# Performance work log

Hardware: AMD Instinct MI355X
Metric: run time of the kernel (lower is better)

## Reference

```python
import jax, jax.numpy as jnp
import numpy as np

S, D, BN, GH, AH, FCH = 18, 512, 32, 128, 16, 512


def setup_inputs() -> dict:
    key = jax.random.key(0)
    ks = jax.random.split(key, 20)
    B = 8192
    sc = 0.05
    inp = {
        "local_styles": jax.random.normal(ks[0], (B, S, D), jnp.float32),
        "global_styles": jax.random.normal(ks[1], (B, S, D), jnp.float32),
        "target_ages": jax.random.uniform(ks[2], (B,), jnp.float32),
        # per-style bottleneck MLPs (512->32->32), stacked over styles
        "bn_w1": jax.random.normal(ks[3], (S, D, BN), jnp.float32) * sc,
        "bn_b1": jnp.zeros((S, BN), jnp.float32),
        "bn_w2": jax.random.normal(ks[4], (S, BN, BN), jnp.float32) * sc,
        "bn_b2": jnp.zeros((S, BN), jnp.float32),
        # global mlp (18*32 -> 128 -> 128)
        "gm_w1": jax.random.normal(ks[5], (S * BN, GH), jnp.float32) * sc,
        "gm_b1": jnp.zeros((GH,), jnp.float32),
        "gm_w2": jax.random.normal(ks[6], (GH, GH), jnp.float32) * sc,
        "gm_b2": jnp.zeros((GH,), jnp.float32),
        # age mlp (1 -> 16 -> 16)
        "age_w1": jax.random.normal(ks[7], (1, AH), jnp.float32) * sc,
        "age_b1": jnp.zeros((AH,), jnp.float32),
        "age_w2": jax.random.normal(ks[8], (AH, AH), jnp.float32) * sc,
        "age_b2": jnp.zeros((AH,), jnp.float32),
        # per-style fc MLPs (128+16+512 -> 512 -> 512), stacked over styles
        "fc_w1": jax.random.normal(ks[9], (S, GH + AH + D, FCH), jnp.float32) * sc,
        "fc_b1": jnp.zeros((S, FCH), jnp.float32),
        "fc_w2": jax.random.normal(ks[10], (S, FCH, D), jnp.float32) * sc,
        "fc_b2": jnp.zeros((S, D), jnp.float32),
    }
    return inp


def reference(local_styles, global_styles, target_ages,
              bn_w1, bn_b1, bn_w2, bn_b2,
              gm_w1, gm_b1, gm_w2, gm_b2,
              age_w1, age_b1, age_w2, age_b2,
              fc_w1, fc_b1, fc_w2, fc_b2):
    B = global_styles.shape[0]
    # per-style bottlenecks as batched GEMMs over the style axis
    h = jax.nn.relu(jnp.einsum('bsd,sdk->bsk', global_styles, bn_w1) + bn_b1)
    h = jnp.einsum('bsk,skm->bsm', h, bn_w2) + bn_b2          # [B, S, 32]
    gf = h.reshape(B, S * BN)                                  # concat over styles
    gf = jax.nn.relu(gf @ gm_w1 + gm_b1) @ gm_w2 + gm_b2      # [B, 128]
    af = target_ages[:, None]                                  # [B, 1]
    af = jax.nn.relu(af @ age_w1 + age_b1) @ age_w2 + age_b2   # [B, 16]
    gfa = jnp.concatenate([gf, af], axis=1)                    # [B, 144]
    # per-style fc: input is [global_feats, style_i] -> [B, S, 656]
    x = jnp.concatenate([jnp.broadcast_to(gfa[:, None, :], (B, S, GH + AH)),
                         global_styles], axis=2)
    y = jax.nn.relu(jnp.einsum('bsf,sfh->bsh', x, fc_w1) + fc_b1)
    y = jnp.einsum('bsh,shd->bsd', y, fc_w2) + fc_b2
    return y + global_styles
```

## Files before the change

### kernel.cpp

```cpp
#include <hip/hip_runtime.h>

typedef unsigned short u16;
typedef unsigned int   u32;
typedef __attribute__((ext_vector_type(4))) float floatx4;
typedef __attribute__((ext_vector_type(8))) short shortx8;

#define BB 8192
#define SS 18
#define DD 512

__device__ __forceinline__ u16 f2bf(float f){
  u32 u = __float_as_uint(f);
  return (u16)((u + 0x7FFFu + ((u >> 16) & 1u)) >> 16);
}
__device__ __forceinline__ float bf2f(u16 x){ return __uint_as_float(((u32)x)<<16); }

__device__ __forceinline__ shortx8 pack8v(floatx4 a, floatx4 b){
  shortx8 t;
  t[0]=(short)f2bf(a[0]); t[1]=(short)f2bf(a[1]); t[2]=(short)f2bf(a[2]); t[3]=(short)f2bf(a[3]);
  t[4]=(short)f2bf(b[0]); t[5]=(short)f2bf(b[1]); t[6]=(short)f2bf(b[2]); t[7]=(short)f2bf(b[3]);
  return t;
}

__device__ __forceinline__ void gload16(const void* g, void* l){
  __builtin_amdgcn_global_load_lds((const __attribute__((address_space(1))) void*)g,
                                   (__attribute__((address_space(3))) void*)l, 16, 0, 0);
}

template<int CALLS>
__device__ __forceinline__ void gstage(const char* src, size_t rowStrideB, int chunkByteOff,
                                       char* lds, int wid, int lane){
#pragma unroll
  for (int i=0;i<CALLS;++i){
    int base = (wid*CALLS + i)*1024;
    int off  = base + lane*16;
    int row  = off >> 7;
    int blk  = ((off >> 4) & 7) ^ (row & 7);
    gload16(src + (size_t)row*rowStrideB + chunkByteOff + blk*16, lds + base);
  }
}

__device__ __forceinline__ void lds_store4(char* buf, int row, int rowBytes, int khByte,
                                           int swzMask, const shortx8* v){
#pragma unroll
  for (int q=0;q<4;++q){
    int off = row*rowBytes + khByte + q*16;
    off ^= (row & swzMask) << 4;
    *(shortx8*)(buf + off) = v[q];
  }
}

__device__ __forceinline__ void stage_bf16(char* buf, const u16* gsrc, size_t srcRowBytes, int tid){
  int row = tid >> 1, kh = tid & 1;
  const char* p = (const char*)gsrc + (size_t)row*srcRowBytes + kh*64;
  shortx8 v[4];
#pragma unroll
  for (int q=0;q<4;++q) v[q] = *(const shortx8*)(p + q*16);
  lds_store4(buf, row, 128, kh*64, 7, v);
}

__device__ __forceinline__ shortx8 lds_frag(const char* buf, int row, int rowBytes, int kByte,
                                            int swzMask, int lane){
  int off = row*rowBytes + kByte + ((lane>>4)<<4);
  off ^= (row & swzMask) << 4;
  return *(const shortx8*)(buf + off);
}

template<int MF, int NF>
__device__ __forceinline__ void mma64(const char* As, const char* Bs, int wm, int wn, int lane,
                                      floatx4 acc[MF][NF]){
#pragma unroll
  for (int kk=0; kk<2; ++kk){
    shortx8 a[MF], b[NF];
#pragma unroll
    for (int i=0;i<MF;++i) a[i] = lds_frag(As, wm + i*16 + (lane&15), 128, kk*64, 7, lane);
#pragma unroll
    for (int j=0;j<NF;++j) b[j] = lds_frag(Bs, wn + j*16 + (lane&15), 128, kk*64, 7, lane);
#pragma unroll
    for (int i=0;i<MF;++i)
#pragma unroll
      for (int j=0;j<NF;++j)
        acc[i][j] = __builtin_amdgcn_mfma_f32_16x16x32_bf16(a[i], b[j], acc[i][j], 0, 0, 0);
  }
}

template<int MF, int NF>
__device__ __forceinline__ void frags_load(const char* As, const char* Bs, int wm, int wn, int lane,
                                           shortx8 a[2][MF], shortx8 b[2][NF]){
#pragma unroll
  for (int kk=0;kk<2;++kk){
#pragma unroll
    for (int i=0;i<MF;++i) a[kk][i] = lds_frag(As, wm + i*16 + (lane&15), 128, kk*64, 7, lane);
#pragma unroll
    for (int j=0;j<NF;++j) b[kk][j] = lds_frag(Bs, wn + j*16 + (lane&15), 128, kk*64, 7, lane);
  }
}
template<int MF, int NF>
__device__ __forceinline__ void frags_mma(shortx8 a[2][MF], shortx8 b[2][NF], floatx4 acc[MF][NF]){
#pragma unroll
  for (int kk=0;kk<2;++kk)
#pragma unroll
    for (int i=0;i<MF;++i)
#pragma unroll
      for (int j=0;j<NF;++j)
        acc[i][j] = __builtin_amdgcn_mfma_f32_16x16x32_bf16(a[kk][i], b[kk][j], acc[i][j], 0, 0, 0);
}

__device__ __forceinline__ int xcd_swz(int bid, int nwg){
  int q = nwg >> 3;
  return (bid & 7)*q + (bid >> 3);
}

__global__ __launch_bounds__(256) void transpose_w2(const float* __restrict__ src,
                                                    u16* __restrict__ dst,
                                                    int sKstride, int kSrcOff, int Kuse,
                                                    int N, int Kpad, int kDstOff){
  __shared__ float tile[32][33];
  int s = blockIdx.z;
  int k0 = blockIdx.x*32, n0 = blockIdx.y*32;
  int tx = threadIdx.x & 31, ty = threadIdx.x >> 5;
#pragma unroll
  for (int r=0;r<4;++r){
    int k = k0 + ty*4 + r;
    float v = (k < Kuse) ? src[((size_t)s*sKstride + kSrcOff + k)*N + n0 + tx] : 0.f;
    tile[ty*4+r][tx] = v;
  }
  __syncthreads();
#pragma unroll
  for (int r=0;r<4;++r){
    int n = n0 + ty*4 + r;
    dst[((size_t)s*N + n)*Kpad + kDstOff + k0 + tx] = f2bf(tile[tx][ty*4+r]);
  }
}

__global__ __launch_bounds__(256) void k_bn(const float* __restrict__ gs,
     const u16* __restrict__ w1t, const u16* __restrict__ w2t,
     const float* __restrict__ b1, const float* __restrict__ b2,
     u16* __restrict__ h2b, u16* __restrict__ gsb){
  __shared__ __align__(16) char SMB[40960];
  int tid = threadIdx.x, lane = tid & 63, wid = tid >> 6;
  int nb = xcd_swz(blockIdx.x, 1152);
  int m0 = (nb & 63)*128, s = nb >> 6;
  floatx4 acc[2][2] = {};
  const char*  Bsrc = (const char*)w1t + (size_t)s*32*1024;
  size_t rowIdx = ((size_t)(m0 + (tid>>1))*SS + s)*DD + (tid&1)*32;
  const float* Ags  = gs + rowIdx;
  u16*         Gsb  = gsb + rowIdx;
  floatx4 fr[8];
  gstage<1>(Bsrc, 1024, 0, SMB+32768, wid, lane);
#pragma unroll
  for (int q=0;q<8;++q) fr[q] = *(const floatx4*)(Ags + q*4);
  for (int c=0;c<8;++c){
    char* Asc = SMB + (c&1)*16384;
    char* Bsc = SMB + 32768 + (c&1)*4096;
    { shortx8 v[4];
#pragma unroll
      for (int q=0;q<4;++q) v[q] = pack8v(fr[2*q], fr[2*q+1]);
      u16* gp = Gsb + c*64;
#pragma unroll
      for (int q=0;q<4;++q) *(shortx8*)(gp + q*8) = v[q];
      lds_store4(Asc, tid>>1, 128, (tid&1)*64, 7, v); }
    __syncthreads();
    int cn = c+1;
    if (cn < 8){
      gstage<1>(Bsrc, 1024, cn*128, SMB + 32768 + (cn&1)*4096, wid, lane);
      const float* p = Ags + cn*64;
#pragma unroll
      for (int q=0;q<8;++q) fr[q] = *(const floatx4*)(p + q*4);
    }
    mma64<2,2>(Asc, Bsc, wid*32, 0, lane, acc);
  }
  __syncthreads();
  char* G1  = SMB;
  char* W2s = SMB + 8192;
#pragma unroll
  for (int i=0;i<2;++i)
#pragma unroll
   for (int j=0;j<2;++j){
    int col = j*16 + (lane&15);
    float bias = b1[s*32 + col];
#pragma unroll
    for (int r=0;r<4;++r){
      int row = wid*32 + i*16 + ((lane>>4)<<2) + r;
      float v = fmaxf(acc[i][j][r] + bias, 0.f);
      int off = (row*64 + col*2) ^ ((row&3)<<4);
      *(u16*)(G1 + off) = f2bf(v);
    }
  }
  if (tid < 32){
    const u16* p = w2t + (size_t)s*32*32 + tid*32;
#pragma unroll
    for (int q=0;q<4;++q){
      int off = (tid*64 + q*16) ^ ((tid&3)<<4);
      *(shortx8*)(W2s + off) = *(const shortx8*)(p + q*8);
    }
  }
  __syncthreads();
  floatx4 acc2[2][2] = {};
  {
    shortx8 a[2], b[2];
#pragma unroll
    for (int i=0;i<2;++i) a[i] = lds_frag(G1,  wid*32 + i*16 + (lane&15), 64, 0, 3, lane);
#pragma unroll
    for (int j=0;j<2;++j) b[j] = lds_frag(W2s, j*16 + (lane&15),          64, 0, 3, lane);
#pragma unroll
    for (int i=0;i<2;++i)
#pragma unroll
      for (int j=0;j<2;++j)
        acc2[i][j] = __builtin_amdgcn_mfma_f32_16x16x32_bf16(a[i], b[j], acc2[i][j], 0,0,0);
  }
#pragma unroll
  for (int i=0;i<2;++i)
#pragma unroll
   for (int j=0;j<2;++j){
    int col = j*16 + (lane&15);
    float bias = b2[s*32 + col];
#pragma unroll
    for (int r=0;r<4;++r){
      int row = wid*32 + i*16 + ((lane>>4)<<2) + r;
      h2b[((size_t)(m0+row)*SS + s)*32 + col] = f2bf(acc2[i][j][r] + bias);
    }
  }
}

__global__ __launch_bounds__(256) void k_gm(const u16* __restrict__ h2b,
     const u16* __restrict__ w1t, const u16* __restrict__ w2t,
     const float* __restrict__ b1, const float* __restrict__ b2,
     const float* __restrict__ ta, const float* __restrict__ aw1, const float* __restrict__ ab1,
     const float* __restrict__ aw2, const float* __restrict__ ab2,
     u16* __restrict__ gfab){
  __shared__ __align__(16) char As[128*128];
  __shared__ __align__(16) char Bs[128*128];
  __shared__ __align__(16) char G1[128*256];
  int tid=threadIdx.x, lane=tid&63, w=tid>>6;
  int m0 = blockIdx.x*128;
  floatx4 acc[2][8] = {};
  for (int c=0;c<9;++c){
    __syncthreads();
    stage_bf16(As, h2b + (size_t)m0*576 + c*64, 1152, tid);
    stage_bf16(Bs, w1t + c*64,                 1152, tid);
    __syncthreads();
    mma64<2,8>(As, Bs, w*32, 0, lane, acc);
  }
#pragma unroll
  for (int i=0;i<2;++i)
#pragma unroll
   for (int j=0;j<8;++j){
    int col = j*16 + (lane&15);
    float bias = b1[col];
#pragma unroll
    for (int r=0;r<4;++r){
      int row = w*32 + i*16 + ((lane>>4)<<2) + r;
      float v = fmaxf(acc[i][j][r] + bias, 0.f);
      int off = (row*256 + col*2) ^ ((row&7)<<4);
      *(u16*)(G1 + off) = f2bf(v);
    }
  }
  floatx4 acc2[2][8] = {};
  for (int c2=0;c2<2;++c2){
    __syncthreads();
    stage_bf16(Bs, w2t + c2*64, 256, tid);
    __syncthreads();
#pragma unroll
    for (int kk=0;kk<2;++kk){
      shortx8 a[2], b[8];
#pragma unroll
      for (int i=0;i<2;++i){
        int row = w*32 + i*16 + (lane&15);
        int off = (row*256 + c2*128 + kk*64 + ((lane>>4)<<4)) ^ ((row&7)<<4);
        a[i] = *(const shortx8*)(G1 + off);
      }
#pragma unroll
      for (int j=0;j<8;++j) b[j] = lds_frag(Bs, j*16 + (lane&15), 128, kk*64, 7, lane);
#pragma unroll
      for (int i=0;i<2;++i)
#pragma unroll
        for (int j=0;j<8;++j)
          acc2[i][j] = __builtin_amdgcn_mfma_f32_16x16x32_bf16(a[i], b[j], acc2[i][j], 0,0,0);
    }
  }
#pragma unroll
  for (int i=0;i<2;++i)
#pragma unroll
   for (int j=0;j<8;++j){
    int col = j*16 + (lane&15);
    float bias = b2[col];
#pragma unroll
    for (int r=0;r<4;++r){
      int row = w*32 + i*16 + ((lane>>4)<<2) + r;
      gfab[(size_t)(m0+row)*192 + col] = f2bf(acc2[i][j][r] + bias);
    }
  }
  if (tid < 128){
    int bidx = m0 + tid;
    float t = ta[bidx];
    float a1[16];
#pragma unroll
    for (int j2=0;j2<16;++j2){ float v = t*aw1[j2] + ab1[j2]; a1[j2] = fmaxf(v, 0.f); }
#pragma unroll
    for (int m=0;m<16;++m){
      float v = ab2[m];
#pragma unroll
      for (int j2=0;j2<16;++j2) v += a1[j2]*aw2[j2*16+m];
      gfab[(size_t)bidx*192 + 128 + m] = f2bf(v);
    }
    shortx8 zz = {};
#pragma unroll
    for (int z=0;z<6;++z) *(shortx8*)(gfab + (size_t)bidx*192 + 144 + z*8) = zz;
  }
}

__global__ __launch_bounds__(256) void k_fc1(const u16* __restrict__ gfab,
     const u16* __restrict__ gsb, const u16* __restrict__ w1t,
     const float* __restrict__ b1, u16* __restrict__ y1b){
  __shared__ __align__(16) char SMB[81920];
  int tid=threadIdx.x, lane=tid&63, wid=tid>>6;
  int nb = xcd_swz(blockIdx.x, 4608);
  int n0=(nb&3)*128, m0=((nb>>2)&63)*128, s=nb>>8;
  int wm=(wid>>1)*64, wn=(wid&1)*64;
  floatx4 acc[4][4] = {};
  const char* Ag   = (const char*)gfab + (size_t)m0*384;
  const char* Agl  = (const char*)gsb + ((size_t)m0*SS + s)*1024;
  const char* Bsrc = (const char*)w1t + ((size_t)s*512+n0)*1408;
#define F1_ISSA(t) do{ int _t=(t); char* _d = SMB + (_t%3)*16384; \
    if (_t<3) gstage<4>(Ag, 384, _t*128, _d, wid, lane); \
    else      gstage<4>(Agl, (size_t)SS*1024, _t*128-384, _d, wid, lane); }while(0)
#define F1_ISSB(t) gstage<4>(Bsrc, 1408, (t)*128, SMB+49152+((t)&1)*16384, wid, lane)
  F1_ISSB(0); F1_ISSA(0); F1_ISSA(1);
#pragma unroll 1
  for (int c=0;c<11;++c){
    if (c<10) asm volatile("s_waitcnt vmcnt(4)" ::: "memory");
    else      asm volatile("s_waitcnt vmcnt(0)" ::: "memory");
    __builtin_amdgcn_s_barrier();
    __builtin_amdgcn_sched_barrier(0);
    shortx8 a[2][4], b[2][4];
    frags_load<4,4>(SMB+(c%3)*16384, SMB+49152+(c&1)*16384, wm, wn, lane, a, b);
    if (c+1<11) F1_ISSB(c+1);
    if (c+2<11) F1_ISSA(c+2);
    frags_mma<4,4>(a, b, acc);
  }
  __syncthreads();
  char* OT = SMB;
#pragma unroll
  for (int i=0;i<4;++i)
#pragma unroll
   for (int j=0;j<4;++j){
    int col = wn + j*16 + (lane&15);
    float bias = b1[(size_t)s*512 + n0 + col];
#pragma unroll
    for (int r=0;r<4;++r){
      int row = wm + i*16 + ((lane>>4)<<2) + r;
      float v = fmaxf(acc[i][j][r] + bias, 0.f);
      int off = (row*256 + col*2) ^ ((row&7)<<4);
      *(u16*)(OT + off) = f2bf(v);
    }
  }
  __syncthreads();
  {
    int row = tid>>1, half = tid&1;
    u16* gp = y1b + ((size_t)(m0+row)*SS + s)*DD + n0 + half*64;
#pragma unroll
    for (int q=0;q<8;++q){
      int off = (row*256 + half*128 + q*16) ^ ((row&7)<<4);
      *(shortx8*)(gp + q*8) = *(const shortx8*)(OT + off);
    }
  }
}

__global__ __launch_bounds__(256) void k_fc2(const u16* __restrict__ y1b,
     const u16* __restrict__ gsb, const u16* __restrict__ w2t,
     const float* __restrict__ b2, float* __restrict__ out){
  __shared__ __align__(16) char SMB[81920];
  int tid=threadIdx.x, lane=tid&63, wid=tid>>6;
  int nb = xcd_swz(blockIdx.x, 4608);
  int n0=(nb&3)*128, m0=((nb>>2)&63)*128, s=nb>>8;
  int wm=(wid>>1)*64, wn=(wid&1)*64;
  floatx4 acc[4][4] = {};
  const char* Asrc = (const char*)y1b + ((size_t)m0*SS + s)*1024;
  const char* Bsrc = (const char*)w2t + ((size_t)s*512 + n0)*1024;
#define F2_ISSA(t) gstage<4>(Asrc, (size_t)SS*1024, (t)*128, SMB+((t)%3)*16384, wid, lane)
#define F2_ISSB(t) gstage<4>(Bsrc, 1024, (t)*128, SMB+49152+((t)&1)*16384, wid, lane)
  F2_ISSB(0); F2_ISSA(0); F2_ISSA(1);
#pragma unroll 1
  for (int c=0;c<8;++c){
    if (c<7) asm volatile("s_waitcnt vmcnt(4)" ::: "memory");
    else     asm volatile("s_waitcnt vmcnt(0)" ::: "memory");
    __builtin_amdgcn_s_barrier();
    __builtin_amdgcn_sched_barrier(0);
    shortx8 a[2][4], b[2][4];
    frags_load<4,4>(SMB+(c%3)*16384, SMB+49152+(c&1)*16384, wm, wn, lane, a, b);
    if (c+1<8) F2_ISSB(c+1);
    if (c+2<8) F2_ISSA(c+2);
    frags_mma<4,4>(a, b, acc);
  }
  __syncthreads();
  float* SMF = (float*)SMB;
#pragma unroll
  for (int i=0;i<4;++i)
#pragma unroll
   for (int j=0;j<4;++j){
    int col = wn + j*16 + (lane&15);
#pragma unroll
    for (int r=0;r<4;++r){
      int row = wm + i*16 + ((lane>>4)<<2) + r;
      int off = (row*512 + col*4) ^ ((row&7)<<4);
      *(float*)((char*)SMF + off) = acc[i][j][r];
    }
  }
  __syncthreads();
  {
    int row = tid>>1, half = tid&1;
    size_t gidx = ((size_t)(m0+row)*SS + s)*DD + n0 + half*64;
    const float* bp = b2 + (size_t)s*512 + n0 + half*64;
    const u16*   gp = gsb + gidx;
#pragma unroll
    for (int q2=0;q2<8;++q2){
      shortx8 gv = *(const shortx8*)(gp + q2*8);
      int off0 = (row*512 + half*256 + (2*q2)*16)   ^ ((row&7)<<4);
      int off1 = (row*512 + half*256 + (2*q2+1)*16) ^ ((row&7)<<4);
      floatx4 v0 = *(const floatx4*)((char*)SMF + off0);
      floatx4 v1 = *(const floatx4*)((char*)SMF + off1);
      floatx4 b0 = *(const floatx4*)(bp + q2*8);
      floatx4 b1v= *(const floatx4*)(bp + q2*8 + 4);
      floatx4 g0, g1;
      g0[0]=bf2f((u16)gv[0]); g0[1]=bf2f((u16)gv[1]); g0[2]=bf2f((u16)gv[2]); g0[3]=bf2f((u16)gv[3]);
      g1[0]=bf2f((u16)gv[4]); g1[1]=bf2f((u16)gv[5]); g1[2]=bf2f((u16)gv[6]); g1[3]=bf2f((u16)gv[7]);
      *(floatx4*)(out + gidx + q2*8)     = v0 + b0 + g0;
      *(floatx4*)(out + gidx + q2*8 + 4) = v1 + b1v + g1;
    }
  }
}

extern "C" void kernel_launch(void* const* d_in, const int* in_sizes, int n_in,
                              void* d_out, int out_size, void* d_ws, size_t ws_size,
                              hipStream_t stream){
  (void)in_sizes; (void)n_in; (void)out_size; (void)ws_size;
  const float* gs   = (const float*)d_in[1];
  const float* ta   = (const float*)d_in[2];
  const float* bnw1 = (const float*)d_in[3];
  const float* bnb1 = (const float*)d_in[4];
  const float* bnw2 = (const float*)d_in[5];
  const float* bnb2 = (const float*)d_in[6];
  const float* gmw1 = (const float*)d_in[7];
  const float* gmb1 = (const float*)d_in[8];
  const float* gmw2 = (const float*)d_in[9];
  const float* gmb2 = (const float*)d_in[10];
  const float* aw1  = (const float*)d_in[11];
  const float* ab1  = (const float*)d_in[12];
  const float* aw2  = (const float*)d_in[13];
  const float* ab2  = (const float*)d_in[14];
  const float* fcw1 = (const float*)d_in[15];
  const float* fcb1 = (const float*)d_in[16];
  const float* fcw2 = (const float*)d_in[17];
  const float* fcb2 = (const float*)d_in[18];

  char* ws = (char*)d_ws;
  u16* fcW1t = (u16*)(ws + 0);
  u16* fcW2t = (u16*)(ws + 12976128);
  u16* bnW1t = (u16*)(ws + 22413312);
  u16* bnW2t = (u16*)(ws + 23003136);
  u16* gmW1t = (u16*)(ws + 23040000);
  u16* gmW2t = (u16*)(ws + 23187456);
  u16* h2b   = (u16*)(ws + 23220224);
  u16* gfab  = (u16*)(ws + 32657408);
  u16* y1b   = (u16*)(ws + 35803136);
  u16* gsb   = (u16*)(ws + 186798080);
  float* out = (float*)d_out;

  dim3 blk(256);
  transpose_w2<<<dim3(16,1,18),  blk, 0, stream>>>(bnw1, bnW1t, 512, 0, 512,  32, 512, 0);
  transpose_w2<<<dim3(1,1,18),   blk, 0, stream>>>(bnw2, bnW2t,  32, 0,  32,  32,  32, 0);
  transpose_w2<<<dim3(18,4,1),   blk, 0, stream>>>(gmw1, gmW1t, 576, 0, 576, 128, 576, 0);
  transpose_w2<<<dim3(4,4,1),    blk, 0, stream>>>(gmw2, gmW2t, 128, 0, 128, 128, 128, 0);
  transpose_w2<<<dim3(6,16,18),  blk, 0, stream>>>(fcw1, fcW1t, 656, 0,   144, 512, 704, 0);
  transpose_w2<<<dim3(16,16,18), blk, 0, stream>>>(fcw1, fcW1t, 656, 144, 512, 512, 704, 192);
  transpose_w2<<<dim3(16,16,18), blk, 0, stream>>>(fcw2, fcW2t, 512, 0, 512, 512, 512, 0);

  k_bn <<<dim3(1152), blk, 0, stream>>>(gs, bnW1t, bnW2t, bnb1, bnb2, h2b, gsb);
  k_gm <<<dim3(64),   blk, 0, stream>>>(h2b, gmW1t, gmW2t, gmb1, gmb2, ta, aw1, ab1, aw2, ab2, gfab);
  k_fc1<<<dim3(4608), blk, 0, stream>>>(gfab, gsb, fcW1t, fcb1, y1b);
  k_fc2<<<dim3(4608), blk, 0, stream>>>(y1b, gsb, fcW2t, fcb2, out);
}
```

Before: 573.4 us.

## Fuse per-style fc1 and fc2 GEMMs into one kernel keeping hidden activations in LDS

Replaces the separate k_fc1 and k_fc2 kernels with a single k_fused kernel that uses 512 threads. Each block takes 64 rows for one style and loops over four 128-wide hidden chunks. It computes relu(x·W1+b1) into LDS, then accumulates that chunk times W2 into register accumulators, and finally adds the bias and residual. This removes the global write and re-read of the large bf16 y1 intermediate and one kernel launch, and it also switches gsb to a style-major layout. In exchange, the smaller M tile means W1 and W2 are streamed again for every 64-row tile. The roughly 148 KB of LDS likely limits occupancy to one block per CU, only one wave issues the A loads, and the epilogue writes scalar floats instead of vectorised stores.

```diff
diff --git a/kernel.cpp b/kernel.cpp
--- a/kernel.cpp
+++ b/kernel.cpp
@@ -82,28 +82,6 @@
       for (int j=0;j<NF;++j)
         acc[i][j] = __builtin_amdgcn_mfma_f32_16x16x32_bf16(a[i], b[j], acc[i][j], 0, 0, 0);
   }
-}
-
-template<int MF, int NF>
-__device__ __forceinline__ void frags_load(const char* As, const char* Bs, int wm, int wn, int lane,
-                                           shortx8 a[2][MF], shortx8 b[2][NF]){
-#pragma unroll
-  for (int kk=0;kk<2;++kk){
-#pragma unroll
-    for (int i=0;i<MF;++i) a[kk][i] = lds_frag(As, wm + i*16 + (lane&15), 128, kk*64, 7, lane);
-#pragma unroll
-    for (int j=0;j<NF;++j) b[kk][j] = lds_frag(Bs, wn + j*16 + (lane&15), 128, kk*64, 7, lane);
-  }
-}
-template<int MF, int NF>
-__device__ __forceinline__ void frags_mma(shortx8 a[2][MF], shortx8 b[2][NF], floatx4 acc[MF][NF]){
-#pragma unroll
-  for (int kk=0;kk<2;++kk)
-#pragma unroll
-    for (int i=0;i<MF;++i)
-#pragma unroll
-      for (int j=0;j<NF;++j)
-        acc[i][j] = __builtin_amdgcn_mfma_f32_16x16x32_bf16(a[kk][i], b[kk][j], acc[i][j], 0, 0, 0);
 }
 
 __device__ __forceinline__ int xcd_swz(int bid, int nwg){
@@ -143,9 +121,8 @@
   int m0 = (nb & 63)*128, s = nb >> 6;
   floatx4 acc[2][2] = {};
   const char*  Bsrc = (const char*)w1t + (size_t)s*32*1024;
-  size_t rowIdx = ((size_t)(m0 + (tid>>1))*SS + s)*DD + (tid&1)*32;
-  const float* Ags  = gs + rowIdx;
-  u16*         Gsb  = gsb + rowIdx;
+  const float* Ags  = gs + ((size_t)(m0 + (tid>>1))*SS + s)*DD + (tid&1)*32;
+  u16*         Gsb  = gsb + ((size_t)s*BB + m0 + (tid>>1))*DD + (tid&1)*32;
   floatx4 fr[8];
   gstage<1>(Bsrc, 1024, 0, SMB+32768, wid, lane);
 #pragma unroll
@@ -310,123 +287,135 @@
   }
 }
 
-__global__ __launch_bounds__(256) void k_fc1(const u16* __restrict__ gfab,
-     const u16* __restrict__ gsb, const u16* __restrict__ w1t,
-     const float* __restrict__ b1, u16* __restrict__ y1b){
-  __shared__ __align__(16) char SMB[81920];
+__global__ __launch_bounds__(512, 2) void k_fused(const u16* __restrict__ gfab,
+     const u16* __restrict__ gsb, const u16* __restrict__ w1t, const u16* __restrict__ w2t,
+     const float* __restrict__ b1, const float* __restrict__ b2, float* __restrict__ out){
+  __shared__ __align__(16) char SMB[151552];
+  char* W1R = SMB;
+  char* W2R = SMB + 24576;
+  char* Y1  = SMB + 122880;
+  char* AR  = SMB + 139264;
   int tid=threadIdx.x, lane=tid&63, wid=tid>>6;
-  int nb = xcd_swz(blockIdx.x, 4608);
-  int n0=(nb&3)*128, m0=((nb>>2)&63)*128, s=nb>>8;
-  int wm=(wid>>1)*64, wn=(wid&1)*64;
-  floatx4 acc[4][4] = {};
-  const char* Ag   = (const char*)gfab + (size_t)m0*384;
-  const char* Agl  = (const char*)gsb + ((size_t)m0*SS + s)*1024;
-  const char* Bsrc = (const char*)w1t + ((size_t)s*512+n0)*1408;
-#define F1_ISSA(t) do{ int _t=(t); char* _d = SMB + (_t%3)*16384; \
-    if (_t<3) gstage<4>(Ag, 384, _t*128, _d, wid, lane); \
-    else      gstage<4>(Agl, (size_t)SS*1024, _t*128-384, _d, wid, lane); }while(0)
-#define F1_ISSB(t) gstage<4>(Bsrc, 1408, (t)*128, SMB+49152+((t)&1)*16384, wid, lane)
-  F1_ISSB(0); F1_ISSA(0); F1_ISSA(1);
+  int nb = xcd_swz(blockIdx.x, 2304);
+  int mt = nb & 127, s = nb >> 7;
+  int m0 = mt*64;
+  int wmRow = (wid>>2)*32;
+  int wn1   = (wid&3)*32;
+  int wd    = (wid&3)*128;
+  floatx4 acc_out[2][8] = {};
+  const char* gA6 = (const char*)gfab + (size_t)m0*384;
+  const char* gAs = (const char*)gsb + ((size_t)s*BB + m0)*1024;
+  const char* gW1 = (const char*)w1t + (size_t)s*512*1408;
+  const char* gW2 = (const char*)w2t + (size_t)s*512*1024;
+
+#define ISSA(tc) do{ if (wid==0){ char* _d = AR + ((tc)%3)*4096; \
+    const char* _s = ((tc)<6) ? (gA6 + (size_t)lane*384 + (tc)*64) \
+                              : (gAs + (size_t)lane*1024 + ((tc)-6)*64); \
+    gload16(_s,      _d +        lane*16); \
+    gload16(_s + 16, _d + 1024 + lane*16); \
+    gload16(_s + 32, _d + 2048 + lane*16); \
+    gload16(_s + 48, _d + 3072 + lane*16); } }while(0)
+#define ISSW1(g, tc) do{ char* _d = W1R + ((tc)%3)*8192 + wid*1024 + lane*16; \
+    int _r = (g)*128 + ((wid&1)<<6) + lane; int _b = wid>>1; \
+    gload16(gW1 + (size_t)_r*1408 + (tc)*64 + _b*16, _d); }while(0)
+#define ISSW2(g, c2) do{ _Pragma("unroll") for (int _i=0;_i<4;++_i){ \
+    int _u = wid*4+_i; char* _d = W2R + ((c2)%3)*32768 + _u*1024 + lane*16; \
+    int _r = ((_u&7)<<6) + lane; int _b = _u>>3; \
+    gload16(gW2 + (size_t)_r*1024 + (g)*256 + (c2)*64 + _b*16, _d); } }while(0)
+
 #pragma unroll 1
-  for (int c=0;c<11;++c){
-    if (c<10) asm volatile("s_waitcnt vmcnt(4)" ::: "memory");
-    else      asm volatile("s_waitcnt vmcnt(0)" ::: "memory");
-    __builtin_amdgcn_s_barrier();
-    __builtin_amdgcn_sched_barrier(0);
-    shortx8 a[2][4], b[2][4];
-    frags_load<4,4>(SMB+(c%3)*16384, SMB+49152+(c&1)*16384, wm, wn, lane, a, b);
-    if (c+1<11) F1_ISSB(c+1);
-    if (c+2<11) F1_ISSA(c+2);
-    frags_mma<4,4>(a, b, acc);
-  }
-  __syncthreads();
-  char* OT = SMB;
-#pragma unroll
-  for (int i=0;i<4;++i)
-#pragma unroll
-   for (int j=0;j<4;++j){
-    int col = wn + j*16 + (lane&15);
-    float bias = b1[(size_t)s*512 + n0 + col];
-#pragma unroll
-    for (int r=0;r<4;++r){
-      int row = wm + i*16 + ((lane>>4)<<2) + r;
-      float v = fmaxf(acc[i][j][r] + bias, 0.f);
-      int off = (row*256 + col*2) ^ ((row&7)<<4);
-      *(u16*)(OT + off) = f2bf(v);
-    }
-  }
-  __syncthreads();
-  {
-    int row = tid>>1, half = tid&1;
-    u16* gp = y1b + ((size_t)(m0+row)*SS + s)*DD + n0 + half*64;
-#pragma unroll
-    for (int q=0;q<8;++q){
-      int off = (row*256 + half*128 + q*16) ^ ((row&7)<<4);
-      *(shortx8*)(gp + q*8) = *(const shortx8*)(OT + off);
-    }
-  }
-}
-
-__global__ __launch_bounds__(256) void k_fc2(const u16* __restrict__ y1b,
-     const u16* __restrict__ gsb, const u16* __restrict__ w2t,
-     const float* __restrict__ b2, float* __restrict__ out){
-  __shared__ __align__(16) char SMB[81920];
-  int tid=threadIdx.x, lane=tid&63, wid=tid>>6;
-  int nb = xcd_swz(blockIdx.x, 4608);
-  int n0=(nb&3)*128, m0=((nb>>2)&63)*128, s=nb>>8;
-  int wm=(wid>>1)*64, wn=(wid&1)*64;
-  floatx4 acc[4][4] = {};
-  const char* Asrc = (const char*)y1b + ((size_t)m0*SS + s)*1024;
-  const char* Bsrc = (const char*)w2t + ((size_t)s*512 + n0)*1024;
-#define F2_ISSA(t) gstage<4>(Asrc, (size_t)SS*1024, (t)*128, SMB+((t)%3)*16384, wid, lane)
-#define F2_ISSB(t) gstage<4>(Bsrc, 1024, (t)*128, SMB+49152+((t)&1)*16384, wid, lane)
-  F2_ISSB(0); F2_ISSA(0); F2_ISSA(1);
-#pragma unroll 1
-  for (int c=0;c<8;++c){
-    if (c<7) asm volatile("s_waitcnt vmcnt(4)" ::: "memory");
-    else     asm volatile("s_waitcnt vmcnt(0)" ::: "memory");
-    __builtin_amdgcn_s_barrier();
-    __builtin_amdgcn_sched_barrier(0);
-    shortx8 a[2][4], b[2][4];
-    frags_load<4,4>(SMB+(c%3)*16384, SMB+49152+(c&1)*16384, wm, wn, lane, a, b);
-    if (c+1<8) F2_ISSB(c+1);
-    if (c+2<8) F2_ISSA(c+2);
-    frags_mma<4,4>(a, b, acc);
-  }
-  __syncthreads();
-  float* SMF = (float*)SMB;
-#pragma unroll
-  for (int i=0;i<4;++i)
-#pragma unroll
-   for (int j=0;j<4;++j){
-    int col = wn + j*16 + (lane&15);
-#pragma unroll
-    for (int r=0;r<4;++r){
-      int row = wm + i*16 + ((lane>>4)<<2) + r;
-      int off = (row*512 + col*4) ^ ((row&7)<<4);
-      *(float*)((char*)SMF + off) = acc[i][j][r];
-    }
-  }
-  __syncthreads();
-  {
-    int row = tid>>1, half = tid&1;
-    size_t gidx = ((size_t)(m0+row)*SS + s)*DD + n0 + half*64;
-    const float* bp = b2 + (size_t)s*512 + n0 + half*64;
-    const u16*   gp = gsb + gidx;
-#pragma unroll
-    for (int q2=0;q2<8;++q2){
-      shortx8 gv = *(const shortx8*)(gp + q2*8);
-      int off0 = (row*512 + half*256 + (2*q2)*16)   ^ ((row&7)<<4);
-      int off1 = (row*512 + half*256 + (2*q2+1)*16) ^ ((row&7)<<4);
-      floatx4 v0 = *(const floatx4*)((char*)SMF + off0);
-      floatx4 v1 = *(const floatx4*)((char*)SMF + off1);
-      floatx4 b0 = *(const floatx4*)(bp + q2*8);
-      floatx4 b1v= *(const floatx4*)(bp + q2*8 + 4);
-      floatx4 g0, g1;
-      g0[0]=bf2f((u16)gv[0]); g0[1]=bf2f((u16)gv[1]); g0[2]=bf2f((u16)gv[2]); g0[3]=bf2f((u16)gv[3]);
-      g1[0]=bf2f((u16)gv[4]); g1[1]=bf2f((u16)gv[5]); g1[2]=bf2f((u16)gv[6]); g1[3]=bf2f((u16)gv[7]);
-      *(floatx4*)(out + gidx + q2*8)     = v0 + b0 + g0;
-      *(floatx4*)(out + gidx + q2*8 + 4) = v1 + b1v + g1;
+  for (int g=0; g<4; ++g){
+    floatx4 acc_y[2][2] = {};
+    ISSA(0); ISSW1(g,0); ISSA(1); ISSW1(g,1);
+#pragma unroll
+    for (int c=0;c<22;++c){
+      if (c<21){ if (wid==0) asm volatile("s_waitcnt vmcnt(5)" ::: "memory");
+                 else        asm volatile("s_waitcnt vmcnt(1)" ::: "memory"); }
+      else       asm volatile("s_waitcnt vmcnt(0)" ::: "memory");
+      __builtin_amdgcn_s_barrier();
+      __builtin_amdgcn_sched_barrier(0);
+      if (c+2<22){ ISSA(c+2); ISSW1(g, c+2); }
+      __builtin_amdgcn_sched_barrier(0);
+      const char* Ab = AR + (c%3)*4096;
+      const char* Bb = W1R + (c%3)*8192;
+      shortx8 a[2], b[2];
+#pragma unroll
+      for (int i=0;i<2;++i){
+        int r = wmRow + i*16 + (lane&15);
+        a[i] = *(const shortx8*)(Ab + ((lane>>4)<<10) + r*16);
+      }
+#pragma unroll
+      for (int j=0;j<2;++j){
+        int r = wn1 + j*16 + (lane&15);
+        b[j] = *(const shortx8*)(Bb + ((lane>>4)<<11) + r*16);
+      }
+      __builtin_amdgcn_s_setprio(1);
+#pragma unroll
+      for (int i=0;i<2;++i)
+#pragma unroll
+        for (int j=0;j<2;++j)
+          acc_y[i][j] = __builtin_amdgcn_mfma_f32_16x16x32_bf16(a[i], b[j], acc_y[i][j], 0,0,0);
+      __builtin_amdgcn_s_setprio(0);
+    }
+    ISSW2(g,0); ISSW2(g,1);
+#pragma unroll
+    for (int i=0;i<2;++i)
+#pragma unroll
+     for (int j=0;j<2;++j){
+      int col = wn1 + j*16 + (lane&15);
+      float bias = b1[(size_t)s*512 + g*128 + col];
+#pragma unroll
+      for (int rr=0;rr<4;++rr){
+        int row = wmRow + i*16 + ((lane>>4)<<2) + rr;
+        float v = fmaxf(acc_y[i][j][rr] + bias, 0.f);
+        int off = row*256 + ((col*2) ^ ((row&7)<<4));
+        *(u16*)(Y1 + off) = f2bf(v);
+      }
+    }
+    __syncthreads();
+#pragma unroll
+    for (int c2=0;c2<4;++c2){
+      if (c2<3) asm volatile("s_waitcnt vmcnt(4)" ::: "memory");
+      else      asm volatile("s_waitcnt vmcnt(0)" ::: "memory");
+      __builtin_amdgcn_s_barrier();
+      __builtin_amdgcn_sched_barrier(0);
+      if (c2+2<4) ISSW2(g, c2+2);
+      __builtin_amdgcn_sched_barrier(0);
+      const char* Bb = W2R + (c2%3)*32768;
+      shortx8 a2[2], b2f[8];
+#pragma unroll
+      for (int i=0;i<2;++i){
+        int row = wmRow + i*16 + (lane&15);
+        int off = row*256 + ((c2*64 + ((lane>>4)<<4)) ^ ((row&7)<<4));
+        a2[i] = *(const shortx8*)(Y1 + off);
+      }
+#pragma unroll
+      for (int j=0;j<8;++j){
+        int r = wd + j*16 + (lane&15);
+        b2f[j] = *(const shortx8*)(Bb + ((lane>>4)<<13) + r*16);
+      }
+      __builtin_amdgcn_s_setprio(1);
+#pragma unroll
+      for (int i=0;i<2;++i)
+#pragma unroll
+        for (int j=0;j<8;++j)
+          acc_out[i][j] = __builtin_amdgcn_mfma_f32_16x16x32_bf16(a2[i], b2f[j], acc_out[i][j], 0,0,0);
+      __builtin_amdgcn_s_setprio(0);
+    }
+  }
+#pragma unroll
+  for (int j=0;j<8;++j){
+    int col = wd + j*16 + (lane&15);
+    float bias = b2[(size_t)s*512 + col];
+#pragma unroll
+    for (int i=0;i<2;++i){
+#pragma unroll
+      for (int rr=0;rr<4;++rr){
+        int row = wmRow + i*16 + ((lane>>4)<<2) + rr;
+        u16 gsv = gsb[((size_t)s*BB + m0 + row)*DD + col];
+        size_t gidx = ((size_t)(m0+row)*SS + s)*DD + col;
+        out[gidx] = acc_out[i][j][rr] + bias + bf2f(gsv);
+      }
     }
   }
 }
@@ -463,7 +452,6 @@
   u16* gmW2t = (u16*)(ws + 23187456);
   u16* h2b   = (u16*)(ws + 23220224);
   u16* gfab  = (u16*)(ws + 32657408);
-  u16* y1b   = (u16*)(ws + 35803136);
   u16* gsb   = (u16*)(ws + 186798080);
   float* out = (float*)d_out;
 
@@ -476,8 +464,7 @@
   transpose_w2<<<dim3(16,16,18), blk, 0, stream>>>(fcw1, fcW1t, 656, 144, 512, 512, 704, 192);
   transpose_w2<<<dim3(16,16,18), blk, 0, stream>>>(fcw2, fcW2t, 512, 0, 512, 512, 512, 0);
 
-  k_bn <<<dim3(1152), blk, 0, stream>>>(gs, bnW1t, bnW2t, bnb1, bnb2, h2b, gsb);
-  k_gm <<<dim3(64),   blk, 0, stream>>>(h2b, gmW1t, gmW2t, gmb1, gmb2, ta, aw1, ab1, aw2, ab2, gfab);
-  k_fc1<<<dim3(4608), blk, 0, stream>>>(gfab, gsb, fcW1t, fcb1, y1b);
-  k_fc2<<<dim3(4608), blk, 0, stream>>>(y1b, gsb, fcW2t, fcb2, out);
-}
+  k_bn   <<<dim3(1152), blk,       0, stream>>>(gs, bnW1t, bnW2t, bnb1, bnb2, h2b, gsb);
+  k_gm   <<<dim3(64),   blk,       0, stream>>>(h2b, gmW1t, gmW2t, gmb1, gmb2, ta, aw1, ab1, aw2, ab2, gfab);
+  k_fused<<<dim3(2304), dim3(512), 0, stream>>>(gfab, gsb, fcW1t, fcW2t, fcb1, fcb2, out);
+}
```

Result: slower. 1.130 ms (+97.0%).
